# Kernel tuning notes

Hardware: AMD Instinct MI355X
Metric: run time of the kernel (lower is better)

Reference implementation:

```python
import jax, jax.numpy as jnp
import numpy as np

N = 8192   # number of nodes / relationships
D = 64     # input_dim == output_dim


def setup_inputs() -> dict:
    key = jax.random.key(0)
    ks = jax.random.split(key, 13)
    s = 0.05
    return {
        "object_features": jax.random.normal(ks[0], (N, D), dtype=jnp.float32),
        "relationship_features": jax.random.normal(ks[1], (N, D), dtype=jnp.float32),
        # sparse-ish 0/1 adjacency, as in the reference usage
        "adjacency_matrix": (jax.random.uniform(ks[2], (N, N)) < 0.05).astype(jnp.float32),
        # nn.Linear params, stored as [in, out] (i.e. torch weight transposed)
        "W_obj": jax.random.normal(ks[3], (D, D), dtype=jnp.float32) * s,
        "b_obj": jax.random.normal(ks[4], (D,), dtype=jnp.float32) * s,
        "W_nobj": jax.random.normal(ks[5], (D, D), dtype=jnp.float32) * s,
        "b_nobj": jax.random.normal(ks[6], (D,), dtype=jnp.float32) * s,
        "W_rel": jax.random.normal(ks[7], (D, D), dtype=jnp.float32) * s,
        "b_rel": jax.random.normal(ks[8], (D,), dtype=jnp.float32) * s,
        "W_skip": jax.random.normal(ks[9], (D, D), dtype=jnp.float32) * s,
        "b_skip": jax.random.normal(ks[10], (D,), dtype=jnp.float32) * s,
        "Wa_w": jax.random.normal(ks[11], (2 * D, 1), dtype=jnp.float32) * s,  # Linear(2D -> 1)
        "Wa_b": jax.random.normal(ks[12], (1,), dtype=jnp.float32) * s,
    }


def reference(object_features, relationship_features, adjacency_matrix,
              W_obj, b_obj, W_nobj, b_nobj, W_rel, b_rel,
              W_skip, b_skip, Wa_w, Wa_b):
    x, r, A = object_features, relationship_features, adjacency_matrix
    d = x.shape[1]

    # message projections (small GEMMs)
    msgs_obj = x @ W_obj + b_obj                      # [N, D]
    msgs_nbr = A.T @ (x @ W_nobj + b_nobj)            # [N, D]
    msgs_rel = r @ W_rel + b_rel                      # [N, D]
    aggregated = msgs_obj + msgs_nbr + msgs_rel       # [N, D]

    # Wa(concat([x_i, r_j])) = x_i @ Wa_w[:d] + r_j @ Wa_w[d:] + Wa_b
    # (avoids materializing the [N, N, 2D] concat the torch code builds)
    sx = x @ Wa_w[:d]                                 # [N, 1] (per row i)
    sr = r @ Wa_w[d:]                                 # [N, 1] (per col j)
    scores = (sx + sr.T + Wa_b) * A                   # [N, N], masked-by-multiply
    attention = jax.nn.softmax(scores, axis=1)        # [N, N]

    # sum_j attn[i, j] * aggregated[i, :]  (exactly the torch broadcast-sum over dim=1)
    attn_agg = jnp.einsum('ij,ik->ik', attention, aggregated)  # [N, D]

    return x @ W_skip + b_skip + attn_agg
```

## Files before the change

kernel.cpp:

```cpp
#include <hip/hip_runtime.h>

typedef __attribute__((ext_vector_type(8))) short short8;
typedef __attribute__((ext_vector_type(4))) float f32x4;

#define NN 8192
#define DD 64

__device__ inline unsigned short f2bf(float f){
  unsigned b = __float_as_uint(f);
  b = (b + 0x7fffu + ((b >> 16) & 1u)) >> 16;
  return (unsigned short)b;
}


__global__ __launch_bounds__(256) void k_proj(
    const float* __restrict__ x, const float* __restrict__ r,
    const float* __restrict__ Wobj,  const float* __restrict__ bobj,
    const float* __restrict__ Wnobj, const float* __restrict__ bnobj,
    const float* __restrict__ Wrel,  const float* __restrict__ brel,
    const float* __restrict__ Wskip, const float* __restrict__ bskip,
    float* __restrict__ accT, unsigned short* __restrict__ yT)
{
  const int i  = blockIdx.x * 256 + threadIdx.x;
  const int d0 = blockIdx.y * 8;

  float xv[DD], rv[DD];
  const float4* xp = (const float4*)(x + i * DD);
  const float4* rp = (const float4*)(r + i * DD);
#pragma unroll
  for (int p = 0; p < 16; p++){
    float4 u = xp[p];
    xv[4*p+0]=u.x; xv[4*p+1]=u.y; xv[4*p+2]=u.z; xv[4*p+3]=u.w;
    float4 v = rp[p];
    rv[4*p+0]=v.x; rv[4*p+1]=v.y; rv[4*p+2]=v.z; rv[4*p+3]=v.w;
  }

  float ay[8], az[8];
#pragma unroll
  for (int t = 0; t < 8; t++){ ay[t] = 0.f; az[t] = 0.f; }

#pragma unroll
  for (int k = 0; k < DD; k++){
    const float xk = xv[k], rk = rv[k];
    const int wb = k * DD + d0;
#pragma unroll
    for (int t = 0; t < 8; t++){
      ay[t] += xk * Wnobj[wb + t];
      az[t] += xk * Wobj [wb + t];
      az[t] += xk * Wskip[wb + t];
      az[t] += rk * Wrel [wb + t];
    }
  }

#pragma unroll
  for (int t = 0; t < 8; t++){
    ay[t] += bnobj[d0 + t];
    az[t] += bobj[d0 + t] + brel[d0 + t] + bskip[d0 + t];
    yT[(d0 + t) * NN + i]   = f2bf(ay[t]);
    accT[(d0 + t) * NN + i] = az[t];
  }
}

#define BN 128
#define KSPLIT 16
#define KCH (NN / KSPLIT)
#define NIT (KCH / 64)

__global__ __launch_bounds__(256) void k_spmm(
    const float* __restrict__ A,
    const unsigned short* __restrict__ yT,
    float* __restrict__ part)
{
  __shared__ short Alds[64 * 128];
  __shared__ short Ylds[64 * 72];

  const int tid  = threadIdx.x;
  const int lane = tid & 63;
  const int wave = tid >> 6;
  const int q    = lane >> 4;
  const int nn   = lane & 15;

  const int j0     = blockIdx.x * BN;
  const int kstart = blockIdx.y * KCH;

  const int c4 = tid & 31;
  const int kr = tid >> 5;
  const int cY = tid & 7;
  const int m0 = tid >> 3;

  uint4 abuf[8], ybuf[2];
  auto gload = [&](int it){
    const int kbase = kstart + it * 64;
#pragma unroll
    for (int p = 0; p < 8; p++)
      abuf[p] = *(const uint4*)(A + (size_t)(kbase + kr + p*8) * NN + j0 + c4 * 4);
#pragma unroll
    for (int p = 0; p < 2; p++)
      ybuf[p] = *(const uint4*)(yT + (m0 + p*32) * NN + kbase + cY * 8);
  };

  f32x4 acc[4][2];
#pragma unroll
  for (int a = 0; a < 4; a++)
#pragma unroll
    for (int b = 0; b < 2; b++)
      acc[a][b] = (f32x4){0.f, 0.f, 0.f, 0.f};

  gload(0);
  for (int it = 0; it < NIT; ++it){
    __syncthreads();
#pragma unroll
    for (int p = 0; p < 8; p++){
      const int kk  = kr + p*8;
      const int key = 2 * (p & 3);
      unsigned lo = (abuf[p].y & 0xFFFF0000u) | (abuf[p].x >> 16);
      unsigned hi = (abuf[p].w & 0xFFFF0000u) | (abuf[p].z >> 16);
      const int off = kk * 128 + (((c4 >> 1) ^ key) * 8) + (c4 & 1) * 4;
      *(uint2*)(&Alds[off]) = make_uint2(lo, hi);
    }
#pragma unroll
    for (int p = 0; p < 2; p++)
      *(uint4*)(&Ylds[(m0 + p*32) * 72 + cY * 8]) = ybuf[p];
    __syncthreads();
    if (it + 1 < NIT) gload(it + 1);

#pragma unroll
    for (int ks = 0; ks < 2; ks++){
      short8 af[4];
#pragma unroll
      for (int mt = 0; mt < 4; mt++)
        af[mt] = *(const short8*)(&Ylds[(mt*16 + nn) * 72 + ks*32 + q*8]);
#pragma unroll
      for (int nt = 0; nt < 2; nt++){
        const int col = wave * 32 + nt * 16 + nn;
        const short* bp = &Alds[(ks*32 + q*8) * 128
                                + (((col >> 3) ^ (2*q)) * 8) + (col & 7)];
        short8 bf;
#pragma unroll
        for (int jj = 0; jj < 8; jj++) bf[jj] = bp[jj * 128];
#pragma unroll
        for (int mt = 0; mt < 4; mt++)
          acc[mt][nt] = __builtin_amdgcn_mfma_f32_16x16x32_bf16(af[mt], bf, acc[mt][nt], 0, 0, 0);
      }
    }
  }

  float* pp = part + (size_t)blockIdx.y * DD * NN;
#pragma unroll
  for (int mt = 0; mt < 4; mt++)
#pragma unroll
    for (int nt = 0; nt < 2; nt++)
#pragma unroll
      for (int v = 0; v < 4; v++){
        const int d   = mt * 16 + q * 4 + v;
        const int col = j0 + wave * 32 + nt * 16 + nn;
        pp[d * NN + col] = acc[mt][nt][v];
      }
}

__global__ __launch_bounds__(256) void k_out(
    const float* __restrict__ accT, const float* __restrict__ part,
    float* __restrict__ out)
{
  __shared__ float t[64][33];
  const int tid = threadIdx.x;
  const int jb  = blockIdx.x * 32;

#pragma unroll
  for (int rep = 0; rep < 8; rep++){
    const int d = rep * 8 + (tid >> 5);
    const int j = tid & 31;
    const size_t base = (size_t)d * NN + jb + j;
    float s = accT[base];
#pragma unroll
    for (int kb = 0; kb < KSPLIT; kb++)
      s += part[(size_t)kb * DD * NN + base];
    t[d][j] = s;
  }
  __syncthreads();
#pragma unroll
  for (int rep = 0; rep < 8; rep++){
    const int j = rep * 4 + (tid >> 6);
    const int d = tid & 63;
    out[(size_t)(jb + j) * DD + d] = t[d][j];
  }
}

extern "C" void kernel_launch(void* const* d_in, const int* in_sizes, int n_in,
                              void* d_out, int out_size, void* d_ws, size_t ws_size,
                              hipStream_t stream) {
  const float* x     = (const float*)d_in[0];
  const float* r     = (const float*)d_in[1];
  const float* A     = (const float*)d_in[2];
  const float* Wobj  = (const float*)d_in[3];
  const float* bobj  = (const float*)d_in[4];
  const float* Wnobj = (const float*)d_in[5];
  const float* bnobj = (const float*)d_in[6];
  const float* Wrel  = (const float*)d_in[7];
  const float* brel  = (const float*)d_in[8];
  const float* Wskip = (const float*)d_in[9];
  const float* bskip = (const float*)d_in[10];

  char* ws = (char*)d_ws;
  float* accT        = (float*)ws;
  unsigned short* yT = (unsigned short*)(ws + (size_t)DD*NN*4);
  float* part        = (float*)(ws + 3u*1024*1024);

  k_proj<<<dim3(32, 8), 256, 0, stream>>>(x, r, Wobj, bobj, Wnobj, bnobj,
                                          Wrel, brel, Wskip, bskip, accT, yT);
  k_spmm<<<dim3(NN / BN, KSPLIT), 256, 0, stream>>>(A, yT, part);
  k_out<<<NN / 32, 256, 0, stream>>>(accT, part, (float*)d_out);
}
```

Before: 416.2 us.

## Double-buffer LDS in spmm, halve K-split, and narrow proj output tiles

The spmm kernel now keeps two LDS buffers. The next tile's global loads are issued before the current tile's MFMA work, and the next buffer is staged after that compute, which removes one barrier per iteration. KSPLIT drops from 16 to 8, so there are fewer partial-sum buffers to write and reduce in k_out but also fewer blocks, which lowers parallelism. The projection kernel computes 4 output columns per thread instead of 8 and loads x/r in 16-element chunks, cutting register pressure while doubling the grid and the number of redundant input reads.

```diff
diff --git a/kernel.cpp b/kernel.cpp
--- a/kernel.cpp
+++ b/kernel.cpp
@@ -22,57 +22,59 @@
     float* __restrict__ accT, unsigned short* __restrict__ yT)
 {
   const int i  = blockIdx.x * 256 + threadIdx.x;
-  const int d0 = blockIdx.y * 8;
-
-  float xv[DD], rv[DD];
-  const float4* xp = (const float4*)(x + i * DD);
-  const float4* rp = (const float4*)(r + i * DD);
-#pragma unroll
-  for (int p = 0; p < 16; p++){
-    float4 u = xp[p];
-    xv[4*p+0]=u.x; xv[4*p+1]=u.y; xv[4*p+2]=u.z; xv[4*p+3]=u.w;
-    float4 v = rp[p];
-    rv[4*p+0]=v.x; rv[4*p+1]=v.y; rv[4*p+2]=v.z; rv[4*p+3]=v.w;
-  }
-
-  float ay[8], az[8];
-#pragma unroll
-  for (int t = 0; t < 8; t++){ ay[t] = 0.f; az[t] = 0.f; }
-
-#pragma unroll
-  for (int k = 0; k < DD; k++){
-    const float xk = xv[k], rk = rv[k];
-    const int wb = k * DD + d0;
-#pragma unroll
-    for (int t = 0; t < 8; t++){
-      ay[t] += xk * Wnobj[wb + t];
-      az[t] += xk * Wobj [wb + t];
-      az[t] += xk * Wskip[wb + t];
-      az[t] += rk * Wrel [wb + t];
-    }
-  }
-
-#pragma unroll
-  for (int t = 0; t < 8; t++){
+  const int d0 = blockIdx.y * 4;
+
+  float ay[4] = {0.f,0.f,0.f,0.f}, az[4] = {0.f,0.f,0.f,0.f};
+  const float4* xp = (const float4*)(x + (size_t)i * DD);
+  const float4* rp = (const float4*)(r + (size_t)i * DD);
+
+#pragma unroll
+  for (int kb = 0; kb < 4; kb++){
+    float xv[16], rv[16];
+#pragma unroll
+    for (int p = 0; p < 4; p++){
+      float4 u = xp[kb*4 + p];
+      xv[4*p+0]=u.x; xv[4*p+1]=u.y; xv[4*p+2]=u.z; xv[4*p+3]=u.w;
+      float4 v = rp[kb*4 + p];
+      rv[4*p+0]=v.x; rv[4*p+1]=v.y; rv[4*p+2]=v.z; rv[4*p+3]=v.w;
+    }
+#pragma unroll
+    for (int kk = 0; kk < 16; kk++){
+      const int wb = (kb*16 + kk) * DD + d0;
+      const float xk = xv[kk], rk = rv[kk];
+#pragma unroll
+      for (int t = 0; t < 4; t++){
+        ay[t] += xk * Wnobj[wb + t];
+        az[t] += xk * Wobj [wb + t];
+        az[t] += xk * Wskip[wb + t];
+        az[t] += rk * Wrel [wb + t];
+      }
+    }
+  }
+
+#pragma unroll
+  for (int t = 0; t < 4; t++){
     ay[t] += bnobj[d0 + t];
     az[t] += bobj[d0 + t] + brel[d0 + t] + bskip[d0 + t];
-    yT[(d0 + t) * NN + i]   = f2bf(ay[t]);
-    accT[(d0 + t) * NN + i] = az[t];
+    yT[(size_t)(d0 + t) * NN + i]   = f2bf(ay[t]);
+    accT[(size_t)(d0 + t) * NN + i] = az[t];
   }
 }
 
 #define BN 128
-#define KSPLIT 16
+#define KSPLIT 8
 #define KCH (NN / KSPLIT)
 #define NIT (KCH / 64)
+#define ASZ (64 * 128)
+#define YSZ (64 * 72)
 
 __global__ __launch_bounds__(256) void k_spmm(
     const float* __restrict__ A,
     const unsigned short* __restrict__ yT,
     float* __restrict__ part)
 {
-  __shared__ short Alds[64 * 128];
-  __shared__ short Ylds[64 * 72];
+  __shared__ short Alds[2 * ASZ];
+  __shared__ short Ylds[2 * YSZ];
 
   const int tid  = threadIdx.x;
   const int lane = tid & 63;
@@ -88,53 +90,64 @@
   const int cY = tid & 7;
   const int m0 = tid >> 3;
 
+  const float* ap          = A  + (size_t)(kstart + kr) * NN + j0 + c4 * 4;
+  const unsigned short* yp = yT + (size_t)m0 * NN + kstart + cY * 8;
+
   uint4 abuf[8], ybuf[2];
-  auto gload = [&](int it){
-    const int kbase = kstart + it * 64;
+  auto gload = [&](){
 #pragma unroll
     for (int p = 0; p < 8; p++)
-      abuf[p] = *(const uint4*)(A + (size_t)(kbase + kr + p*8) * NN + j0 + c4 * 4);
+      abuf[p] = *(const uint4*)(ap + (size_t)p * 8 * NN);
 #pragma unroll
     for (int p = 0; p < 2; p++)
-      ybuf[p] = *(const uint4*)(yT + (m0 + p*32) * NN + kbase + cY * 8);
+      ybuf[p] = *(const uint4*)(yp + (size_t)p * 32 * NN);
+    ap += 64 * NN;
+    yp += 64;
   };
-
-  f32x4 acc[4][2];
-#pragma unroll
-  for (int a = 0; a < 4; a++)
-#pragma unroll
-    for (int b = 0; b < 2; b++)
-      acc[a][b] = (f32x4){0.f, 0.f, 0.f, 0.f};
-
-  gload(0);
-  for (int it = 0; it < NIT; ++it){
-    __syncthreads();
+  auto stage = [&](int buf){
+    short* Ab = &Alds[buf * ASZ];
+    short* Yb = &Ylds[buf * YSZ];
 #pragma unroll
     for (int p = 0; p < 8; p++){
       const int kk  = kr + p*8;
       const int key = 2 * (p & 3);
       unsigned lo = (abuf[p].y & 0xFFFF0000u) | (abuf[p].x >> 16);
       unsigned hi = (abuf[p].w & 0xFFFF0000u) | (abuf[p].z >> 16);
-      const int off = kk * 128 + (((c4 >> 1) ^ key) * 8) + (c4 & 1) * 4;
-      *(uint2*)(&Alds[off]) = make_uint2(lo, hi);
+      *(uint2*)(&Ab[kk * 128 + (((c4 >> 1) ^ key) * 8) + (c4 & 1) * 4]) =
+          make_uint2(lo, hi);
     }
 #pragma unroll
     for (int p = 0; p < 2; p++)
-      *(uint4*)(&Ylds[(m0 + p*32) * 72 + cY * 8]) = ybuf[p];
-    __syncthreads();
-    if (it + 1 < NIT) gload(it + 1);
+      *(uint4*)(&Yb[(m0 + p*32) * 72 + cY * 8]) = ybuf[p];
+  };
+
+  f32x4 acc[4][2];
+#pragma unroll
+  for (int a = 0; a < 4; a++)
+#pragma unroll
+    for (int b = 0; b < 2; b++)
+      acc[a][b] = (f32x4){0.f, 0.f, 0.f, 0.f};
+
+  gload();
+  stage(0);
+  __syncthreads();
+
+  for (int it = 0; it < NIT; ++it){
+    if (it + 1 < NIT) gload();
+    const short* Ab = &Alds[(it & 1) * ASZ];
+    const short* Yb = &Ylds[(it & 1) * YSZ];
 
 #pragma unroll
     for (int ks = 0; ks < 2; ks++){
       short8 af[4];
 #pragma unroll
       for (int mt = 0; mt < 4; mt++)
-        af[mt] = *(const short8*)(&Ylds[(mt*16 + nn) * 72 + ks*32 + q*8]);
+        af[mt] = *(const short8*)(&Yb[(mt*16 + nn) * 72 + ks*32 + q*8]);
 #pragma unroll
       for (int nt = 0; nt < 2; nt++){
         const int col = wave * 32 + nt * 16 + nn;
-        const short* bp = &Alds[(ks*32 + q*8) * 128
-                                + (((col >> 3) ^ (2*q)) * 8) + (col & 7)];
+        const short* bp = &Ab[(ks*32 + q*8) * 128
+                              + (((col >> 3) ^ (2*q)) * 8) + (col & 7)];
         short8 bf;
 #pragma unroll
         for (int jj = 0; jj < 8; jj++) bf[jj] = bp[jj * 128];
@@ -143,6 +156,11 @@
           acc[mt][nt] = __builtin_amdgcn_mfma_f32_16x16x32_bf16(af[mt], bf, acc[mt][nt], 0, 0, 0);
       }
     }
+
+    if (it + 1 < NIT){
+      stage((it + 1) & 1);
+      __syncthreads();
+    }
   }
 
   float* pp = part + (size_t)blockIdx.y * DD * NN;
@@ -154,7 +172,7 @@
       for (int v = 0; v < 4; v++){
         const int d   = mt * 16 + q * 4 + v;
         const int col = j0 + wave * 32 + nt * 16 + nn;
-        pp[d * NN + col] = acc[mt][nt][v];
+        pp[(size_t)d * NN + col] = acc[mt][nt][v];
       }
 }
 
@@ -206,8 +224,8 @@
   unsigned short* yT = (unsigned short*)(ws + (size_t)DD*NN*4);
   float* part        = (float*)(ws + 3u*1024*1024);
 
-  k_proj<<<dim3(32, 8), 256, 0, stream>>>(x, r, Wobj, bobj, Wnobj, bnobj,
-                                          Wrel, brel, Wskip, bskip, accT, yT);
+  k_proj<<<dim3(32, 16), 256, 0, stream>>>(x, r, Wobj, bobj, Wnobj, bnobj,
+                                           Wrel, brel, Wskip, bskip, accT, yT);
   k_spmm<<<dim3(NN / BN, KSPLIT), 256, 0, stream>>>(A, yT, part);
   k_out<<<NN / 32, 256, 0, stream>>>(accT, part, (float*)d_out);
 }
```

Result: no change. 414.5 us (-0.4%).
